# Kernel optimization log

Measured on AMD Instinct MI355X. Metric: run time of the kernel, lower is better.

The kernel has to match this reference:

```python
import jax, jax.numpy as jnp
import numpy as np

DEGREES = [1, 2, 3]
NUM_SEGMENTS = len(DEGREES)


def setup_inputs() -> dict:
    key = jax.random.key(0)
    B = 4_000_000
    m_tot = sum(2 * l + 1 for l in DEGREES)  # 15
    sphc = jax.random.normal(key, (B, m_tot), dtype=jnp.float32)
    # Clebsch-Gordan diagonal for l_out=0: a constant per degree block
    # (real-basis value 1/sqrt(2l+1) per m-component), tiled per degree,
    # mirroring the cg_rep buffer built in __init__.
    cg_rep = jnp.concatenate([
        jnp.full((2 * l + 1,), 1.0 / np.sqrt(2 * l + 1), dtype=jnp.float32)
        for l in DEGREES
    ])
    # segment n repeated (2*degrees[n]+1) times -> contiguous sorted blocks
    segment_ids = jnp.concatenate([
        jnp.full((2 * l + 1,), n, dtype=jnp.int32)
        for n, l in enumerate(DEGREES)
    ])
    return {"sphc": sphc, "cg_rep": cg_rep, "segment_ids": segment_ids}


def reference(sphc, cg_rep, segment_ids):
    # (B, m_tot): fused elementwise square * CG weight
    weighted = sphc * sphc * cg_rep[None, :]
    # Per-degree block reduction along the feature axis. Segments are
    # contiguous and sorted, so segment_sum over the transposed feature
    # axis is a direct tiled block reduction (no atomic scatter needed).
    out = jax.ops.segment_sum(
        weighted.T, segment_ids, num_segments=NUM_SEGMENTS,
        indices_are_sorted=True,
    ).T  # (B, num_segments)
    return out
```

## Files before the change

kernel.cpp:

```cpp
#include <hip/hip_runtime.h>
#include <hip/hip_bf16.h>


constexpr int M = 15;
constexpr int NSEG = 3;
constexpr int RPB = 256;
constexpr int IN_F4 = RPB * M / 4;
constexpr int OUT_F4 = RPB * NSEG / 4;

typedef float f32x4 __attribute__((ext_vector_type(4)));

__global__ __launch_bounds__(RPB)
void l0_contract_kernel(const float* __restrict__ sphc,
                        const float* __restrict__ cg_rep,
                        float* __restrict__ out,
                        int B) {
    __shared__ float s_in[RPB * M];
    __shared__ float s_out[RPB * NSEG];

    const int tid = threadIdx.x;
    const long long rowStart = (long long)blockIdx.x * RPB;
    const long long rowsLeft = (long long)B - rowStart;
    const int rowsHere = rowsLeft >= RPB ? RPB : (int)rowsLeft;

    if (rowsHere == RPB) {
        const f32x4* __restrict__ g4 = (const f32x4*)(sphc + rowStart * M);
        f32x4* l4 = (f32x4*)s_in;
#pragma unroll
        for (int k = 0; k < 3; ++k) {
            l4[tid + k * RPB] = g4[tid + k * RPB];
        }
        if (tid < IN_F4 - 3 * RPB) {
            l4[tid + 3 * RPB] = g4[tid + 3 * RPB];
        }
    } else {
        const int n = rowsHere * M;
        const float* g = sphc + rowStart * M;
        for (int i = tid; i < n; i += RPB) s_in[i] = g[i];
    }
    __syncthreads();

    const float c1 = cg_rep[0];
    const float c2 = cg_rep[3];
    const float c3 = cg_rep[8];

    if (tid < rowsHere) {
        const float* r = s_in + tid * M;
        float a = r[0] * r[0] + r[1] * r[1] + r[2] * r[2];
        float b = r[3] * r[3] + r[4] * r[4] + r[5] * r[5]
                + r[6] * r[6] + r[7] * r[7];
        float c = r[8] * r[8] + r[9] * r[9] + r[10] * r[10]
                + r[11] * r[11] + r[12] * r[12] + r[13] * r[13]
                + r[14] * r[14];
        s_out[tid * NSEG + 0] = a * c1;
        s_out[tid * NSEG + 1] = b * c2;
        s_out[tid * NSEG + 2] = c * c3;
    }
    __syncthreads();

    if (rowsHere == RPB) {
        const f32x4* lo4 = (const f32x4*)s_out;
        f32x4* o4 = (f32x4*)(out + rowStart * NSEG);
        if (tid < OUT_F4) {
            __builtin_nontemporal_store(lo4[tid], &o4[tid]);
        }
    } else {
        const int n = rowsHere * NSEG;
        float* o = out + rowStart * NSEG;
        for (int i = tid; i < n; i += RPB) {
            __builtin_nontemporal_store(s_out[i], &o[i]);
        }
    }
}

extern "C" void kernel_launch(void* const* d_in, const int* in_sizes, int n_in,
                              void* d_out, int out_size, void* d_ws, size_t ws_size,
                              hipStream_t stream) {
    const float* sphc   = (const float*)d_in[0];
    const float* cg_rep = (const float*)d_in[1];
    float* out = (float*)d_out;

    const int B = in_sizes[0] / M;
    const int grid = (B + RPB - 1) / RPB;

    l0_contract_kernel<<<grid, RPB, 0, stream>>>(sphc, cg_rep, out, B);
}
```

Before: 337.2 us.

## Use a persistent grid-stride kernel that prefetches the next tile into registers

Replaces the one-tile-per-block launch with a persistent kernel of at most 2048 blocks. Each block loops over tiles and issues the global loads for the next tile into registers while it computes the current tile from LDS. Any partial last tile is handled by a separate simple per-row tail kernel. The aim is to overlap memory latency with compute and reduce block scheduling overhead, at the cost of higher register use and fewer resident blocks than a full-size grid.

```diff
diff --git a/kernel.cpp b/kernel.cpp
--- a/kernel.cpp
+++ b/kernel.cpp
@@ -5,72 +5,93 @@
 constexpr int M = 15;
 constexpr int NSEG = 3;
 constexpr int RPB = 256;
+constexpr int BLK = 256;
 constexpr int IN_F4 = RPB * M / 4;
 constexpr int OUT_F4 = RPB * NSEG / 4;
 
 typedef float f32x4 __attribute__((ext_vector_type(4)));
 
-__global__ __launch_bounds__(RPB)
-void l0_contract_kernel(const float* __restrict__ sphc,
-                        const float* __restrict__ cg_rep,
-                        float* __restrict__ out,
-                        int B) {
+__global__ __launch_bounds__(BLK)
+void l0_contract_pipe(const float* __restrict__ sphc,
+                      const float* __restrict__ cg_rep,
+                      float* __restrict__ out,
+                      int nTiles) {
     __shared__ float s_in[RPB * M];
     __shared__ float s_out[RPB * NSEG];
 
     const int tid = threadIdx.x;
-    const long long rowStart = (long long)blockIdx.x * RPB;
-    const long long rowsLeft = (long long)B - rowStart;
-    const int rowsHere = rowsLeft >= RPB ? RPB : (int)rowsLeft;
-
-    if (rowsHere == RPB) {
-        const f32x4* __restrict__ g4 = (const f32x4*)(sphc + rowStart * M);
-        f32x4* l4 = (f32x4*)s_in;
-#pragma unroll
-        for (int k = 0; k < 3; ++k) {
-            l4[tid + k * RPB] = g4[tid + k * RPB];
-        }
-        if (tid < IN_F4 - 3 * RPB) {
-            l4[tid + 3 * RPB] = g4[tid + 3 * RPB];
-        }
-    } else {
-        const int n = rowsHere * M;
-        const float* g = sphc + rowStart * M;
-        for (int i = tid; i < n; i += RPB) s_in[i] = g[i];
-    }
-    __syncthreads();
-
     const float c1 = cg_rep[0];
     const float c2 = cg_rep[3];
     const float c3 = cg_rep[8];
 
-    if (tid < rowsHere) {
-        const float* r = s_in + tid * M;
-        float a = r[0] * r[0] + r[1] * r[1] + r[2] * r[2];
-        float b = r[3] * r[3] + r[4] * r[4] + r[5] * r[5]
-                + r[6] * r[6] + r[7] * r[7];
-        float c = r[8] * r[8] + r[9] * r[9] + r[10] * r[10]
-                + r[11] * r[11] + r[12] * r[12] + r[13] * r[13]
-                + r[14] * r[14];
-        s_out[tid * NSEG + 0] = a * c1;
-        s_out[tid * NSEG + 1] = b * c2;
-        s_out[tid * NSEG + 2] = c * c3;
+    int tile = blockIdx.x;
+    if (tile >= nTiles) return;
+
+    f32x4 v0, v1, v2, v3;
+    {
+        const f32x4* __restrict__ g4 = (const f32x4*)sphc + (long long)tile * IN_F4;
+        v0 = g4[tid];
+        v1 = g4[tid + 256];
+        v2 = g4[tid + 512];
+        if (tid < IN_F4 - 768) v3 = g4[tid + 768];
     }
-    __syncthreads();
 
-    if (rowsHere == RPB) {
-        const f32x4* lo4 = (const f32x4*)s_out;
-        f32x4* o4 = (f32x4*)(out + rowStart * NSEG);
+    for (;;) {
+        f32x4* l4 = (f32x4*)s_in;
+        l4[tid]       = v0;
+        l4[tid + 256] = v1;
+        l4[tid + 512] = v2;
+        if (tid < IN_F4 - 768) l4[tid + 768] = v3;
+        __syncthreads();
+
+        const int next = tile + gridDim.x;
+        if (next < nTiles) {
+            const f32x4* __restrict__ gn = (const f32x4*)sphc + (long long)next * IN_F4;
+            v0 = gn[tid];
+            v1 = gn[tid + 256];
+            v2 = gn[tid + 512];
+            if (tid < IN_F4 - 768) v3 = gn[tid + 768];
+        }
+
+        {
+            const float* r = s_in + tid * M;
+            float a = r[0] * r[0] + r[1] * r[1] + r[2] * r[2];
+            float b = r[3] * r[3] + r[4] * r[4] + r[5] * r[5]
+                    + r[6] * r[6] + r[7] * r[7];
+            float c = r[8] * r[8] + r[9] * r[9] + r[10] * r[10]
+                    + r[11] * r[11] + r[12] * r[12] + r[13] * r[13]
+                    + r[14] * r[14];
+            s_out[tid * NSEG + 0] = a * c1;
+            s_out[tid * NSEG + 1] = b * c2;
+            s_out[tid * NSEG + 2] = c * c3;
+        }
+        __syncthreads();
+
         if (tid < OUT_F4) {
+            const f32x4* lo4 = (const f32x4*)s_out;
+            f32x4* o4 = (f32x4*)out + (long long)tile * OUT_F4;
             __builtin_nontemporal_store(lo4[tid], &o4[tid]);
         }
-    } else {
-        const int n = rowsHere * NSEG;
-        float* o = out + rowStart * NSEG;
-        for (int i = tid; i < n; i += RPB) {
-            __builtin_nontemporal_store(s_out[i], &o[i]);
-        }
+
+        if (next >= nTiles) break;
+        tile = next;
     }
+}
+
+__global__ void l0_contract_tail(const float* __restrict__ sphc,
+                                 const float* __restrict__ cg_rep,
+                                 float* __restrict__ out,
+                                 int startRow, int B) {
+    const int r = startRow + blockIdx.x * blockDim.x + threadIdx.x;
+    if (r >= B) return;
+    const float c1 = cg_rep[0], c2 = cg_rep[3], c3 = cg_rep[8];
+    const float* x = sphc + (long long)r * M;
+    float a = x[0]*x[0] + x[1]*x[1] + x[2]*x[2];
+    float b = x[3]*x[3] + x[4]*x[4] + x[5]*x[5] + x[6]*x[6] + x[7]*x[7];
+    float c = x[8]*x[8] + x[9]*x[9] + x[10]*x[10] + x[11]*x[11]
+            + x[12]*x[12] + x[13]*x[13] + x[14]*x[14];
+    float* o = out + (long long)r * NSEG;
+    o[0] = a * c1; o[1] = b * c2; o[2] = c * c3;
 }
 
 extern "C" void kernel_launch(void* const* d_in, const int* in_sizes, int n_in,
@@ -81,7 +102,16 @@
     float* out = (float*)d_out;
 
     const int B = in_sizes[0] / M;
-    const int grid = (B + RPB - 1) / RPB;
+    const int nTiles = B / RPB;
+    const int rem = B - nTiles * RPB;
 
-    l0_contract_kernel<<<grid, RPB, 0, stream>>>(sphc, cg_rep, out, B);
+    const int GRID = 2048;
+    const int grid = nTiles < GRID ? nTiles : GRID;
+    if (nTiles > 0) {
+        l0_contract_pipe<<<grid, BLK, 0, stream>>>(sphc, cg_rep, out, nTiles);
+    }
+    if (rem > 0) {
+        l0_contract_tail<<<(rem + 255) / 256, 256, 0, stream>>>(
+            sphc, cg_rep, out, nTiles * RPB, B);
+    }
 }
```

Result: no change. 340.3 us (+0.9%).
